# Kernel optimization log

Hardware: AMD Instinct MI355X
Metric: run time of the kernel (lower is better)

## Reference

```python
import jax, jax.numpy as jnp
import numpy as np

D = 64       # link_state_dim
RU = 256     # readout_units
N = 50000    # num_edges (total links)
E = 800000   # number of (main, neighbour) message pairs
K_PATHS = 8
T_STEPS = 3


def setup_inputs() -> dict:
    key = jax.random.key(0)
    ks = jax.random.split(key, 10)
    std = 0.1  # init_weight uses normal(std=0.1) for Linear/GRUCell weights
    return {
        'links_state': jax.random.normal(ks[0], (N, D), dtype=jnp.float32),
        'id_mainEdges': jax.random.randint(ks[1], (E,), 0, N),
        'id_neighbourEdges': jax.random.randint(ks[2], (E,), 0, N),
        'W_msg': std * jax.random.normal(ks[3], (D, 2 * D), dtype=jnp.float32),
        'b_msg': jnp.zeros((D,), jnp.float32),
        'W_ih': std * jax.random.normal(ks[4], (3 * D, D), dtype=jnp.float32),
        'W_hh': std * jax.random.normal(ks[5], (3 * D, D), dtype=jnp.float32),
        'b_ih': jnp.zeros((3 * D,), jnp.float32),
        'b_hh': jnp.zeros((3 * D,), jnp.float32),
        'Wr1': std * jax.random.normal(ks[6], (RU, D), dtype=jnp.float32),
        'br1': jnp.zeros((RU,), jnp.float32),
        'Wr2': std * jax.random.normal(ks[7], (RU, RU), dtype=jnp.float32),
        'br2': jnp.zeros((RU,), jnp.float32),
        'Wr3': std * jax.random.normal(ks[8], (1, RU), dtype=jnp.float32),
        'br3': jnp.zeros((1,), jnp.float32),
        'K': K_PATHS,
        'T': T_STEPS,
        'num_edges': N,
    }


def _gru_cell(x, h, W_ih, W_hh, b_ih, b_hh):
    gi = x @ W_ih.T + b_ih            # [N, 3D]
    gh = h @ W_hh.T + b_hh            # [N, 3D]
    i_r, i_z, i_n = jnp.split(gi, 3, axis=1)
    h_r, h_z, h_n = jnp.split(gh, 3, axis=1)
    r = jax.nn.sigmoid(i_r + h_r)
    z = jax.nn.sigmoid(i_z + h_z)
    n = jnp.tanh(i_n + r * h_n)
    return (1.0 - z) * n + z * h


def reference(links_state, id_mainEdges, id_neighbourEdges, W_msg, b_msg,
              W_ih, W_hh, b_ih, b_hh, Wr1, br1, Wr2, br2, Wr3, br3,
              K, T, num_edges):
    for _ in range(T):  # fixed small message-passing depth
        # gather + concat: [E, 2D]
        cat = jnp.concatenate([links_state[id_mainEdges],
                               links_state[id_neighbourEdges]], axis=1)
        m = jax.nn.selu(cat @ W_msg.T + b_msg)                       # [E, D]
        links_M = jax.ops.segment_sum(m, id_neighbourEdges,
                                      num_segments=num_edges)        # [N, D]
        links_state = _gru_cell(links_M, links_state, W_ih, W_hh, b_ih, b_hh)
    # group edges into K paths (contiguous blocks, per K_paths_ids construction)
    per_path = num_edges // K
    path_ids = jnp.arange(num_edges) // per_path
    k_path_outputs = jax.ops.segment_sum(links_state, path_ids,
                                         num_segments=K)             # [K, D]
    h = jax.nn.selu(k_path_outputs @ Wr1.T + br1)
    h = jax.nn.selu(h @ Wr2.T + br2)
    logits = (h @ Wr3.T + br3).reshape(-1)                           # [K]
    return jax.nn.softmax(logits)  # Categorical probs over K paths
```

## Files before the change

kernel.cpp:

```cpp
#include <hip/hip_runtime.h>
#include <hip/hip_bf16.h>

#define D 64
#define CAP 5120

typedef _Float16 f16;
typedef _Float16 f16x2 __attribute__((ext_vector_type(2)));
typedef _Float16 f16x4 __attribute__((ext_vector_type(4)));
typedef _Float16 f16x8 __attribute__((ext_vector_type(8)));
typedef float f32x16 __attribute__((ext_vector_type(16)));

#define MFMA_F16(a, b, c) __builtin_amdgcn_mfma_f32_32x32x16_f16(a, b, c, 0, 0, 0)

__device__ __forceinline__ float selu_f(float x) {
    const float SC = 1.0507009873554805f;
    const float AL = 1.6732632423543772f;
    return x > 0.f ? SC * x : SC * AL * (__expf(x) - 1.f);
}
__device__ __forceinline__ float sigmoid_f(float x) { return 1.f / (1.f + __expf(-x)); }
__device__ __forceinline__ float tanh_f(float x) {
    float s = x < 0.f ? -1.f : 1.f;
    float t = __expf(-2.f * fabsf(x));
    return s * (1.f - t) / (1.f + t);
}
__device__ __forceinline__ float dot4(float4 a, float4 b, float acc) {
    acc = fmaf(a.x, b.x, acc);
    acc = fmaf(a.y, b.y, acc);
    acc = fmaf(a.z, b.z, acc);
    return fmaf(a.w, b.w, acc);
}
__device__ __forceinline__ f32x16 zero16() {
    f32x16 v;
#pragma unroll
    for (int i = 0; i < 16; ++i) v[i] = 0.f;
    return v;
}

__global__ void __launch_bounds__(256) pack_kernel(const float* __restrict__ Wih,
                                                   const float* __restrict__ Whh,
                                                   const float* __restrict__ Wmsg,
                                                   f16* __restrict__ w16,
                                                   float* __restrict__ kp) {
    int idx = blockIdx.x * 256 + threadIdx.x;
    if (idx < 512) kp[idx] = 0.f;
    int g = idx >> 12;
    int rem = idx & 4095;
    int d = rem >> 6, k0 = rem & 63;
    float v;
    if (g < 3)      v = Wih[(g * 64 + d) * 64 + k0];
    else if (g < 6) v = Whh[((g - 3) * 64 + d) * 64 + k0];
    else            v = Wmsg[d * 128 + (g - 6) * 64 + k0];
    w16[g * 4096 + d * 64 + (k0 ^ ((d & 7) << 3))] = (f16)v;
}

__global__ void __launch_bounds__(256) bucket_kernel(const int* __restrict__ idm,
                                                     const int* __restrict__ idn,
                                                     int* __restrict__ cursor,
                                                     uint2* __restrict__ barr,
                                                     int E, int NBK) {
    __shared__ int hist[256];
    __shared__ int gbase[256];
    __shared__ int loff[256];
    int t = threadIdx.x;
    if (t < NBK) hist[t] = 0;
    __syncthreads();
    int tile = blockIdx.x * 2048;
    int n_[8], m_[8], b_[8];
#pragma unroll
    for (int j = 0; j < 8; ++j) {
        int e = tile + j * 256 + t;
        if (e < E) {
            n_[j] = idn[e];
            m_[j] = idm[e];
            b_[j] = n_[j] >> 8;
            atomicAdd(&hist[b_[j]], 1);
        } else {
            b_[j] = -1;
        }
    }
    __syncthreads();
    if (t < NBK) {
        gbase[t] = hist[t] ? atomicAdd(&cursor[t], hist[t]) : 0;
        loff[t] = 0;
    }
    __syncthreads();
#pragma unroll
    for (int j = 0; j < 8; ++j) {
        if (b_[j] >= 0) {
            int r = atomicAdd(&loff[b_[j]], 1);
            uint2 e;
            e.x = (unsigned)n_[j];
            e.y = (unsigned)m_[j];
            barr[(size_t)b_[j] * CAP + gbase[b_[j]] + r] = e;
        }
    }
}

__global__ void __launch_bounds__(256) csr_kernel(const uint2* __restrict__ barr,
                                                  const int* __restrict__ cursor,
                                                  int* __restrict__ row_start,
                                                  int* __restrict__ csr_src,
                                                  int N, int E) {
    __shared__ int hist[256];
    __shared__ int offs[256];
    __shared__ int curc[256];
    __shared__ int red[256];
    __shared__ int ldsIdm[CAP];
    __shared__ int baseSh;
    int b = blockIdx.x, t = threadIdx.x;
    int cntb = cursor[b];
    red[t] = (t < b) ? cursor[t] : 0;
    __syncthreads();
    for (int off = 128; off > 0; off >>= 1) {
        if (t < off) red[t] += red[t + off];
        __syncthreads();
    }
    if (t == 0) baseSh = red[0];
    hist[t] = 0;
    __syncthreads();
    int base = baseSh;
    for (int i = t; i < cntb; i += 256) {
        int n = (int)(barr[(size_t)b * CAP + i].x) & 255;
        atomicAdd(&hist[n], 1);
    }
    __syncthreads();
    int v0 = hist[t];
    offs[t] = v0;
    __syncthreads();
    for (int off = 1; off < 256; off <<= 1) {
        int v = offs[t];
        int u = (t >= off) ? offs[t - off] : 0;
        __syncthreads();
        offs[t] = v + u;
        __syncthreads();
    }
    int excl = offs[t] - v0;
    curc[t] = excl;
    int node = (b << 8) + t;
    if (node < N) row_start[node] = base + excl;
    if (b == gridDim.x - 1 && t == 0) row_start[N] = E;
    __syncthreads();
    for (int i = t; i < cntb; i += 256) {
        uint2 e = barr[(size_t)b * CAP + i];
        int r = atomicAdd(&curc[e.x & 255], 1);
        ldsIdm[r] = (int)e.y;
    }
    __syncthreads();
    for (int i = t; i < cntb; i += 256) csr_src[base + i] = ldsIdm[i];
}

__global__ void __launch_bounds__(256) gather_kernel(
    const f16* __restrict__ y16, const f16* __restrict__ z16,
    const float* __restrict__ bmsg, const int* __restrict__ row_start,
    const int* __restrict__ csr_src, f16* __restrict__ M16, int N) {
    int lane = threadIdx.x & 63;
    int sub = lane >> 5;
    int d0 = (lane & 31) * 2;
    int wave = blockIdx.x * (blockDim.x >> 6) + (threadIdx.x >> 6);
    int nwaves = gridDim.x * (blockDim.x >> 6);
    float b0 = bmsg[d0], b1 = bmsg[d0 + 1];
    for (int i = wave; i < N; i += nwaves) {
        f16x2 zv = *(const f16x2*)&z16[(size_t)i * 64 + d0];
        float zb0 = (float)zv[0] + b0;
        float zb1 = (float)zv[1] + b1;
        int s1 = row_start[i + 1];
        float m0 = 0.f, m1 = 0.f;
        int s = row_start[i] + sub;
        for (; s + 6 < s1; s += 8) {
            int e0 = csr_src[s],     e1 = csr_src[s + 2];
            int e2 = csr_src[s + 4], e3 = csr_src[s + 6];
            f16x2 v0 = *(const f16x2*)&y16[(size_t)e0 * 64 + d0];
            f16x2 v1 = *(const f16x2*)&y16[(size_t)e1 * 64 + d0];
            f16x2 v2 = *(const f16x2*)&y16[(size_t)e2 * 64 + d0];
            f16x2 v3 = *(const f16x2*)&y16[(size_t)e3 * 64 + d0];
            m0 += selu_f((float)v0[0] + zb0);
            m1 += selu_f((float)v0[1] + zb1);
            m0 += selu_f((float)v1[0] + zb0);
            m1 += selu_f((float)v1[1] + zb1);
            m0 += selu_f((float)v2[0] + zb0);
            m1 += selu_f((float)v2[1] + zb1);
            m0 += selu_f((float)v3[0] + zb0);
            m1 += selu_f((float)v3[1] + zb1);
        }
        for (; s < s1; s += 2) {
            int e0 = csr_src[s];
            f16x2 v0 = *(const f16x2*)&y16[(size_t)e0 * 64 + d0];
            m0 += selu_f((float)v0[0] + zb0);
            m1 += selu_f((float)v0[1] + zb1);
        }
        m0 += __shfl_xor(m0, 32, 64);
        m1 += __shfl_xor(m1, 32, 64);
        if (sub == 0) {
            f16x2 mv; mv[0] = (f16)m0; mv[1] = (f16)m1;
            *(f16x2*)&M16[(size_t)i * 64 + d0] = mv;
        }
    }
}

__global__ void __launch_bounds__(256, 2) yz0_kernel(
    const float* __restrict__ x, const f16* __restrict__ w16,
    f16* __restrict__ y16, f16* __restrict__ z16, int N, int NT) {
    __shared__ __align__(16) f16 wlds[2 * 4096];
    __shared__ __align__(16) f16 xh[64 * 64];
    int t = threadIdx.x;
#pragma unroll
    for (int it = 0; it < 4; ++it) {
        int idx = (it * 256 + t) * 8;
        *(f16x8*)&wlds[idx] = *(const f16x8*)&w16[6 * 4096 + idx];
    }
    int lane = t & 63;
    int w = t >> 6;
    int ng = w >> 1;
    int dh = w & 1;
    int arow = ng * 32 + (lane & 31);
    int arow64 = arow * 64;
    int axor = (arow & 7) << 3;
    int bcol = dh * 32 + (lane & 31);
    int bxor = (bcol & 7) << 3;
    int kg = (lane >> 5) * 8;
    __syncthreads();
    for (int tile = blockIdx.x; tile < NT; tile += gridDim.x) {
        int base = tile * 64;
#pragma unroll
        for (int it = 0; it < 4; ++it) {
            int idx = it * 256 + t;
            int node = idx >> 4, k0 = (idx & 15) * 4;
            int gn = base + node;
            f16x4 v;
            if (gn < N) {
                float4 f4 = *(const float4*)&x[(size_t)gn * 64 + k0];
                v[0] = (f16)f4.x; v[1] = (f16)f4.y; v[2] = (f16)f4.z; v[3] = (f16)f4.w;
            } else {
#pragma unroll
                for (int u = 0; u < 4; ++u) v[u] = (f16)0.f;
            }
            *(f16x4*)&xh[node * 64 + (k0 ^ ((node & 7) << 3))] = v;
        }
        __syncthreads();
        f32x16 aY = zero16(), aZ = zero16();
#pragma unroll
        for (int ks = 0; ks < 4; ++ks) {
            int kb = ks * 16 + kg;
            f16x8 ah = *(const f16x8*)&xh[arow64 + (kb ^ axor)];
            int wof = bcol * 64 + (kb ^ bxor);
            aY = MFMA_F16(ah, *(const f16x8*)&wlds[0 * 4096 + wof], aY);
            aZ = MFMA_F16(ah, *(const f16x8*)&wlds[1 * 4096 + wof], aZ);
        }
#pragma unroll
        for (int r = 0; r < 16; ++r) {
            int rowC = (r & 3) + 8 * (r >> 2) + 4 * (lane >> 5);
            int gn = base + ng * 32 + rowC;
            if (gn < N) {
                size_t o = (size_t)gn * 64 + bcol;
                y16[o] = (f16)aY[r];
                z16[o] = (f16)aZ[r];
            }
        }
        __syncthreads();
    }
}

__global__ void __launch_bounds__(256, 2) gruyz_kernel(
    const f16* __restrict__ M16, const float* __restrict__ hin,
    float* __restrict__ hout,
    const float* __restrict__ bih, const float* __restrict__ bhh,
    const f16* __restrict__ w16, f16* __restrict__ y16, f16* __restrict__ z16,
    int N, int NT, int doYZ) {
    __shared__ __align__(16) f16 wlds[8 * 4096];
    __shared__ __align__(16) f16 xm[64 * 64];
    __shared__ __align__(16) f16 xh[64 * 64];
    int t = threadIdx.x;
#pragma unroll 4
    for (int it = 0; it < 16; ++it) {
        int idx = (it * 256 + t) * 8;
        *(f16x8*)&wlds[idx] = *(const f16x8*)&w16[idx];
    }
    int lane = t & 63;
    int w = t >> 6;
    int ng = w >> 1;
    int dh = w & 1;
    int arow = ng * 32 + (lane & 31);
    int arow64 = arow * 64;
    int axor = (arow & 7) << 3;
    int bcol = dh * 32 + (lane & 31);
    int bxor = (bcol & 7) << 3;
    int kg = (lane >> 5) * 8;
    float bIR = bih[bcol], bIZ = bih[64 + bcol], bIN = bih[128 + bcol];
    float bHR = bhh[bcol], bHZ = bhh[64 + bcol], bHN = bhh[128 + bcol];
    __syncthreads();
    for (int tile = blockIdx.x; tile < NT; tile += gridDim.x) {
        int base = tile * 64;
#pragma unroll
        for (int it = 0; it < 2; ++it) {
            int idx = it * 256 + t;
            int node = idx >> 3, k0 = (idx & 7) * 8;
            int gn = base + node;
            f16x8 v;
            if (gn < N) v = *(const f16x8*)&M16[(size_t)gn * 64 + k0];
            else {
#pragma unroll
            for (int u = 0; u < 8; ++u) v[u] = (f16)0.f;
            }
            *(f16x8*)&xm[node * 64 + (k0 ^ ((node & 7) << 3))] = v;
        }
#pragma unroll
        for (int it = 0; it < 4; ++it) {
            int idx = it * 256 + t;
            int node = idx >> 4, k0 = (idx & 15) * 4;
            int gn = base + node;
            f16x4 v;
            if (gn < N) {
                float4 f4 = *(const float4*)&hin[(size_t)gn * 64 + k0];
                v[0] = (f16)f4.x; v[1] = (f16)f4.y; v[2] = (f16)f4.z; v[3] = (f16)f4.w;
            } else {
#pragma unroll
                for (int u = 0; u < 4; ++u) v[u] = (f16)0.f;
            }
            *(f16x4*)&xh[node * 64 + (k0 ^ ((node & 7) << 3))] = v;
        }
        __syncthreads();

        f32x16 aIR = zero16(), aIZ = zero16(), aIN = zero16();
        f32x16 aHR = zero16(), aHZ = zero16(), aHN = zero16();
#pragma unroll
        for (int ks = 0; ks < 4; ++ks) {
            int kb = ks * 16 + kg;
            f16x8 am = *(const f16x8*)&xm[arow64 + (kb ^ axor)];
            f16x8 ah = *(const f16x8*)&xh[arow64 + (kb ^ axor)];
            int wof = bcol * 64 + (kb ^ bxor);
            aIR = MFMA_F16(am, *(const f16x8*)&wlds[0 * 4096 + wof], aIR);
            aIZ = MFMA_F16(am, *(const f16x8*)&wlds[1 * 4096 + wof], aIZ);
            aIN = MFMA_F16(am, *(const f16x8*)&wlds[2 * 4096 + wof], aIN);
            aHR = MFMA_F16(ah, *(const f16x8*)&wlds[3 * 4096 + wof], aHR);
            aHZ = MFMA_F16(ah, *(const f16x8*)&wlds[4 * 4096 + wof], aHZ);
            aHN = MFMA_F16(ah, *(const f16x8*)&wlds[5 * 4096 + wof], aHN);
        }
        __syncthreads();

#pragma unroll
        for (int r = 0; r < 16; ++r) {
            int rowC = (r & 3) + 8 * (r >> 2) + 4 * (lane >> 5);
            int nodeLocal = ng * 32 + rowC;
            int gn = base + nodeLocal;
            float hnew = 0.f;
            if (gn < N) {
                size_t o = (size_t)gn * 64 + bcol;
                float hold = hin[o];
                float rr = sigmoid_f(aIR[r] + bIR + aHR[r] + bHR);
                float zz = sigmoid_f(aIZ[r] + bIZ + aHZ[r] + bHZ);
                float nn = tanh_f(aIN[r] + bIN + rr * (aHN[r] + bHN));
                hnew = (1.f - zz) * nn + zz * hold;
                hout[o] = hnew;
            }
            if (doYZ) xm[nodeLocal * 64 + (bcol ^ ((rowC & 7) << 3))] = (f16)hnew;
        }
        if (doYZ) {
            __syncthreads();
            f32x16 aY = zero16(), aZ = zero16();
#pragma unroll
            for (int ks = 0; ks < 4; ++ks) {
                int kb = ks * 16 + kg;
                f16x8 ahn2 = *(const f16x8*)&xm[arow64 + (kb ^ axor)];
                int wof = bcol * 64 + (kb ^ bxor);
                aY = MFMA_F16(ahn2, *(const f16x8*)&wlds[6 * 4096 + wof], aY);
                aZ = MFMA_F16(ahn2, *(const f16x8*)&wlds[7 * 4096 + wof], aZ);
            }
#pragma unroll
            for (int r = 0; r < 16; ++r) {
                int rowC = (r & 3) + 8 * (r >> 2) + 4 * (lane >> 5);
                int gn = base + ng * 32 + rowC;
                if (gn < N) {
                    size_t o = (size_t)gn * 64 + bcol;
                    y16[o] = (f16)aY[r];
                    z16[o] = (f16)aZ[r];
                }
            }
        }
        __syncthreads();
    }
}

__global__ void __launch_bounds__(256) pathsum_kernel(const float* __restrict__ h,
                                                      float* __restrict__ kp, int N, int K) {
    int per = N / K;
    int blocksPerPath = gridDim.x / K;
    int p = blockIdx.x / blocksPerPath;
    int c = blockIdx.x % blocksPerPath;
    int d = threadIdx.x & 63;
    int row0 = c * (blockDim.x >> 6) + (threadIdx.x >> 6);
    int stride = blocksPerPath * (blockDim.x >> 6);
    float acc = 0.f;
    for (int r = row0; r < per; r += stride) acc += h[((size_t)p * per + r) * 64 + d];
    __shared__ float red[256];
    red[threadIdx.x] = acc;
    __syncthreads();
    if (threadIdx.x < 64) {
        float s = red[threadIdx.x] + red[64 + threadIdx.x] + red[128 + threadIdx.x] +
                  red[192 + threadIdx.x];
        atomicAdd(&kp[p * 64 + threadIdx.x], s);
    }
}

__global__ void __launch_bounds__(256) readout1_kernel(const float* __restrict__ kp,
                                                       const float* __restrict__ Wr1,
                                                       const float* __restrict__ br1,
                                                       const float* __restrict__ Wr2,
                                                       const float* __restrict__ br2,
                                                       float* __restrict__ h2) {
    int p = blockIdx.x;
    int t = threadIdx.x;
    __shared__ __align__(16) float kps[64];
    __shared__ __align__(16) float h1[256];
    if (t < 64) kps[t] = kp[p * 64 + t];
    __syncthreads();
    float acc = br1[t];
#pragma unroll
    for (int d4 = 0; d4 < 16; ++d4) {
        float4 wv = *(const float4*)&Wr1[t * 64 + d4 * 4];
        float4 kv = *(const float4*)&kps[d4 * 4];
        acc = dot4(wv, kv, acc);
    }
    h1[t] = selu_f(acc);
    __syncthreads();
    float acc2 = br2[t];
#pragma unroll 8
    for (int j4 = 0; j4 < 64; ++j4) {
        float4 wv = *(const float4*)&Wr2[t * 256 + j4 * 4];
        float4 hv = *(const float4*)&h1[j4 * 4];
        acc2 = dot4(wv, hv, acc2);
    }
    h2[p * 256 + t] = selu_f(acc2);
}

__global__ void __launch_bounds__(256) readout2_kernel(const float* __restrict__ h2,
                                                       const float* __restrict__ Wr3,
                                                       const float* __restrict__ br3,
                                                       float* __restrict__ out) {
    __shared__ float red[256];
    __shared__ float lg[8];
    int t = threadIdx.x;
    float w3 = Wr3[t];
    for (int p = 0; p < 8; ++p) {
        red[t] = w3 * h2[p * 256 + t];
        __syncthreads();
        for (int off = 128; off > 0; off >>= 1) {
            if (t < off) red[t] += red[t + off];
            __syncthreads();
        }
        if (t == 0) lg[p] = red[0] + br3[0];
        __syncthreads();
    }
    if (t == 0) {
        float mx = lg[0];
        for (int p = 1; p < 8; ++p) mx = fmaxf(mx, lg[p]);
        float s = 0.f, e[8];
        for (int p = 0; p < 8; ++p) {
            e[p] = expf(lg[p] - mx);
            s += e[p];
        }
        for (int p = 0; p < 8; ++p) out[p] = e[p] / s;
    }
}

extern "C" void kernel_launch(void* const* d_in, const int* in_sizes, int n_in,
                              void* d_out, int out_size, void* d_ws, size_t ws_size,
                              hipStream_t stream) {
    const float* links_state = (const float*)d_in[0];
    const int* idm = (const int*)d_in[1];
    const int* idn = (const int*)d_in[2];
    const float* Wmsg = (const float*)d_in[3];
    const float* bmsg = (const float*)d_in[4];
    const float* Wih = (const float*)d_in[5];
    const float* Whh = (const float*)d_in[6];
    const float* bih = (const float*)d_in[7];
    const float* bhh = (const float*)d_in[8];
    const float* Wr1 = (const float*)d_in[9];
    const float* br1 = (const float*)d_in[10];
    const float* Wr2 = (const float*)d_in[11];
    const float* br2 = (const float*)d_in[12];
    const float* Wr3 = (const float*)d_in[13];
    const float* br3 = (const float*)d_in[14];

    const int N = in_sizes[0] / D;
    const int E = in_sizes[1];
    const int K = 8, T = 3;
    const int NBK = (N + 255) >> 8;
    const int NT = (N + 63) / 64;

    float* ws = (float*)d_ws;
    size_t nd = (size_t)N * D;
    float* cur = ws;
    f16* y16 = (f16*)(ws + nd);
    f16* z16 = y16 + nd;
    f16* M16 = z16 + nd;
    float* kp = (float*)(M16 + nd);
    float* h2 = kp + 512;
    f16* w16 = (f16*)(h2 + 2048);
    uint2* barr = (uint2*)(w16 + 32768);
    int* ibase = (int*)(barr + (size_t)NBK * CAP);
    int* cursor = ibase;
    int* row_start = ibase + 256;
    int* csr_src = row_start + N + 1;

    hipMemsetAsync(cursor, 0, 256 * sizeof(int), stream);
    bucket_kernel<<<dim3((E + 2047) / 2048), dim3(256), 0, stream>>>(idm, idn, cursor, barr,
                                                                     E, NBK);
    csr_kernel<<<dim3(NBK), dim3(256), 0, stream>>>(barr, cursor, row_start, csr_src, N, E);
    pack_kernel<<<dim3(128), dim3(256), 0, stream>>>(Wih, Whh, Wmsg, w16, kp);

    yz0_kernel<<<dim3(512), dim3(256), 0, stream>>>(links_state, w16, y16, z16, N, NT);
    for (int t = 0; t < T; ++t) {
        gather_kernel<<<dim3(2048), dim3(256), 0, stream>>>(y16, z16, bmsg, row_start,
                                                            csr_src, M16, N);
        gruyz_kernel<<<dim3(512), dim3(256), 0, stream>>>(
            M16, (t == 0) ? links_state : cur, cur, bih, bhh, w16, y16, z16, N, NT,
            t < T - 1 ? 1 : 0);
    }

    pathsum_kernel<<<dim3(256), dim3(256), 0, stream>>>(cur, kp, N, K);
    readout1_kernel<<<dim3(8), dim3(256), 0, stream>>>(kp, Wr1, br1, Wr2, br2, h2);
    readout2_kernel<<<dim3(1), dim3(256), 0, stream>>>(h2, Wr3, br3, (float*)d_out);
}
```

Before: 228.2 us.

## Merge setup, path-sum and readout kernels to cut launch count

Weight packing now runs as extra blocks of the bucket kernel, and the yz0 projection runs as extra blocks of the CSR-build kernel. The path sum moves into the last GRU step through per-tile LDS atomics followed by global atomics. The two readout kernels become one, where the last block to finish does the softmax, using a counter and threadfence. This removes several small launches and a full reread of the final state. The cost is more global atomics, a last-block handshake, and larger LDS use in the merged CSR/yz0 kernel, which may lower occupancy.

After: 215.5 us. -5.5%, faster.

```diff
diff --git a/kernel.cpp b/kernel.cpp
--- a/kernel.cpp
+++ b/kernel.cpp
@@ -36,32 +36,31 @@
     return v;
 }
 
-__global__ void __launch_bounds__(256) pack_kernel(const float* __restrict__ Wih,
-                                                   const float* __restrict__ Whh,
-                                                   const float* __restrict__ Wmsg,
-                                                   f16* __restrict__ w16,
-                                                   float* __restrict__ kp) {
-    int idx = blockIdx.x * 256 + threadIdx.x;
-    if (idx < 512) kp[idx] = 0.f;
-    int g = idx >> 12;
-    int rem = idx & 4095;
-    int d = rem >> 6, k0 = rem & 63;
-    float v;
-    if (g < 3)      v = Wih[(g * 64 + d) * 64 + k0];
-    else if (g < 6) v = Whh[((g - 3) * 64 + d) * 64 + k0];
-    else            v = Wmsg[d * 128 + (g - 6) * 64 + k0];
-    w16[g * 4096 + d * 64 + (k0 ^ ((d & 7) << 3))] = (f16)v;
-}
-
-__global__ void __launch_bounds__(256) bucket_kernel(const int* __restrict__ idm,
-                                                     const int* __restrict__ idn,
-                                                     int* __restrict__ cursor,
-                                                     uint2* __restrict__ barr,
-                                                     int E, int NBK) {
+__global__ void __launch_bounds__(256) bucketpack_kernel(
+    const int* __restrict__ idm, const int* __restrict__ idn,
+    int* __restrict__ cursor, uint2* __restrict__ barr,
+    const float* __restrict__ Wih, const float* __restrict__ Whh,
+    const float* __restrict__ Wmsg, f16* __restrict__ w16,
+    float* __restrict__ kp, int* __restrict__ rdcnt,
+    int E, int NBK, int NBB) {
     __shared__ int hist[256];
     __shared__ int gbase[256];
     __shared__ int loff[256];
     int t = threadIdx.x;
+    if ((int)blockIdx.x >= NBB) {
+        int idx = ((int)blockIdx.x - NBB) * 256 + t;
+        if (idx < 512) kp[idx] = 0.f;
+        if (idx == 0) *rdcnt = 0;
+        int g = idx >> 12;
+        int rem = idx & 4095;
+        int d = rem >> 6, k0 = rem & 63;
+        float v;
+        if (g < 3)      v = Wih[(g * 64 + d) * 64 + k0];
+        else if (g < 6) v = Whh[((g - 3) * 64 + d) * 64 + k0];
+        else            v = Wmsg[d * 128 + (g - 6) * 64 + k0];
+        w16[g * 4096 + d * 64 + (k0 ^ ((d & 7) << 3))] = (f16)v;
+        return;
+    }
     if (t < NBK) hist[t] = 0;
     __syncthreads();
     int tile = blockIdx.x * 2048;
@@ -96,57 +95,120 @@
     }
 }
 
-__global__ void __launch_bounds__(256) csr_kernel(const uint2* __restrict__ barr,
-                                                  const int* __restrict__ cursor,
-                                                  int* __restrict__ row_start,
-                                                  int* __restrict__ csr_src,
-                                                  int N, int E) {
+__global__ void __launch_bounds__(256) csryz0_kernel(
+    const uint2* __restrict__ barr, const int* __restrict__ cursor,
+    int* __restrict__ row_start, int* __restrict__ csr_src,
+    const float* __restrict__ x, const f16* __restrict__ w16,
+    f16* __restrict__ y16, f16* __restrict__ z16,
+    int N, int E, int NT, int NBK, int YZGRID) {
     __shared__ int hist[256];
     __shared__ int offs[256];
     __shared__ int curc[256];
     __shared__ int red[256];
     __shared__ int ldsIdm[CAP];
     __shared__ int baseSh;
-    int b = blockIdx.x, t = threadIdx.x;
-    int cntb = cursor[b];
-    red[t] = (t < b) ? cursor[t] : 0;
-    __syncthreads();
-    for (int off = 128; off > 0; off >>= 1) {
-        if (t < off) red[t] += red[t + off];
-        __syncthreads();
-    }
-    if (t == 0) baseSh = red[0];
-    hist[t] = 0;
-    __syncthreads();
-    int base = baseSh;
-    for (int i = t; i < cntb; i += 256) {
-        int n = (int)(barr[(size_t)b * CAP + i].x) & 255;
-        atomicAdd(&hist[n], 1);
-    }
-    __syncthreads();
-    int v0 = hist[t];
-    offs[t] = v0;
-    __syncthreads();
-    for (int off = 1; off < 256; off <<= 1) {
-        int v = offs[t];
-        int u = (t >= off) ? offs[t - off] : 0;
-        __syncthreads();
-        offs[t] = v + u;
-        __syncthreads();
-    }
-    int excl = offs[t] - v0;
-    curc[t] = excl;
-    int node = (b << 8) + t;
-    if (node < N) row_start[node] = base + excl;
-    if (b == gridDim.x - 1 && t == 0) row_start[N] = E;
-    __syncthreads();
-    for (int i = t; i < cntb; i += 256) {
-        uint2 e = barr[(size_t)b * CAP + i];
-        int r = atomicAdd(&curc[e.x & 255], 1);
-        ldsIdm[r] = (int)e.y;
-    }
-    __syncthreads();
-    for (int i = t; i < cntb; i += 256) csr_src[base + i] = ldsIdm[i];
+    __shared__ __align__(16) f16 wlds[2 * 4096];
+    __shared__ __align__(16) f16 xh[64 * 64];
+    int t = threadIdx.x;
+    if ((int)blockIdx.x < NBK) {
+        int b = blockIdx.x;
+        int cntb = cursor[b];
+        red[t] = (t < b) ? cursor[t] : 0;
+        __syncthreads();
+        for (int off = 128; off > 0; off >>= 1) {
+            if (t < off) red[t] += red[t + off];
+            __syncthreads();
+        }
+        if (t == 0) baseSh = red[0];
+        hist[t] = 0;
+        __syncthreads();
+        int base = baseSh;
+        for (int i = t; i < cntb; i += 256) {
+            int n = (int)(barr[(size_t)b * CAP + i].x) & 255;
+            atomicAdd(&hist[n], 1);
+        }
+        __syncthreads();
+        int v0 = hist[t];
+        offs[t] = v0;
+        __syncthreads();
+        for (int off = 1; off < 256; off <<= 1) {
+            int v = offs[t];
+            int u = (t >= off) ? offs[t - off] : 0;
+            __syncthreads();
+            offs[t] = v + u;
+            __syncthreads();
+        }
+        int excl = offs[t] - v0;
+        curc[t] = excl;
+        int node = (b << 8) + t;
+        if (node < N) row_start[node] = base + excl;
+        if (b == NBK - 1 && t == 0) row_start[N] = E;
+        __syncthreads();
+        for (int i = t; i < cntb; i += 256) {
+            uint2 e = barr[(size_t)b * CAP + i];
+            int r = atomicAdd(&curc[e.x & 255], 1);
+            ldsIdm[r] = (int)e.y;
+        }
+        __syncthreads();
+        for (int i = t; i < cntb; i += 256) csr_src[base + i] = ldsIdm[i];
+        return;
+    }
+    int yb = (int)blockIdx.x - NBK;
+#pragma unroll
+    for (int it = 0; it < 4; ++it) {
+        int idx = (it * 256 + t) * 8;
+        *(f16x8*)&wlds[idx] = *(const f16x8*)&w16[6 * 4096 + idx];
+    }
+    int lane = t & 63;
+    int w = t >> 6;
+    int ng = w >> 1;
+    int dh = w & 1;
+    int arow = ng * 32 + (lane & 31);
+    int arow64 = arow * 64;
+    int axor = (arow & 7) << 3;
+    int bcol = dh * 32 + (lane & 31);
+    int bxor = (bcol & 7) << 3;
+    int kg = (lane >> 5) * 8;
+    __syncthreads();
+    for (int tile = yb; tile < NT; tile += YZGRID) {
+        int base = tile * 64;
+#pragma unroll
+        for (int it = 0; it < 4; ++it) {
+            int idx = it * 256 + t;
+            int node = idx >> 4, k0 = (idx & 15) * 4;
+            int gn = base + node;
+            f16x4 v;
+            if (gn < N) {
+                float4 f4 = *(const float4*)&x[(size_t)gn * 64 + k0];
+                v[0] = (f16)f4.x; v[1] = (f16)f4.y; v[2] = (f16)f4.z; v[3] = (f16)f4.w;
+            } else {
+#pragma unroll
+                for (int u = 0; u < 4; ++u) v[u] = (f16)0.f;
+            }
+            *(f16x4*)&xh[node * 64 + (k0 ^ ((node & 7) << 3))] = v;
+        }
+        __syncthreads();
+        f32x16 aY = zero16(), aZ = zero16();
+#pragma unroll
+        for (int ks = 0; ks < 4; ++ks) {
+            int kb = ks * 16 + kg;
+            f16x8 ah = *(const f16x8*)&xh[arow64 + (kb ^ axor)];
+            int wof = bcol * 64 + (kb ^ bxor);
+            aY = MFMA_F16(ah, *(const f16x8*)&wlds[0 * 4096 + wof], aY);
+            aZ = MFMA_F16(ah, *(const f16x8*)&wlds[1 * 4096 + wof], aZ);
+        }
+#pragma unroll
+        for (int r = 0; r < 16; ++r) {
+            int rowC = (r & 3) + 8 * (r >> 2) + 4 * (lane >> 5);
+            int gn = base + ng * 32 + rowC;
+            if (gn < N) {
+                size_t o = (size_t)gn * 64 + bcol;
+                y16[o] = (f16)aY[r];
+                z16[o] = (f16)aZ[r];
+            }
+        }
+        __syncthreads();
+    }
 }
 
 __global__ void __launch_bounds__(256) gather_kernel(
@@ -197,75 +259,12 @@
     }
 }
 
-__global__ void __launch_bounds__(256, 2) yz0_kernel(
-    const float* __restrict__ x, const f16* __restrict__ w16,
-    f16* __restrict__ y16, f16* __restrict__ z16, int N, int NT) {
-    __shared__ __align__(16) f16 wlds[2 * 4096];
-    __shared__ __align__(16) f16 xh[64 * 64];
-    int t = threadIdx.x;
-#pragma unroll
-    for (int it = 0; it < 4; ++it) {
-        int idx = (it * 256 + t) * 8;
-        *(f16x8*)&wlds[idx] = *(const f16x8*)&w16[6 * 4096 + idx];
-    }
-    int lane = t & 63;
-    int w = t >> 6;
-    int ng = w >> 1;
-    int dh = w & 1;
-    int arow = ng * 32 + (lane & 31);
-    int arow64 = arow * 64;
-    int axor = (arow & 7) << 3;
-    int bcol = dh * 32 + (lane & 31);
-    int bxor = (bcol & 7) << 3;
-    int kg = (lane >> 5) * 8;
-    __syncthreads();
-    for (int tile = blockIdx.x; tile < NT; tile += gridDim.x) {
-        int base = tile * 64;
-#pragma unroll
-        for (int it = 0; it < 4; ++it) {
-            int idx = it * 256 + t;
-            int node = idx >> 4, k0 = (idx & 15) * 4;
-            int gn = base + node;
-            f16x4 v;
-            if (gn < N) {
-                float4 f4 = *(const float4*)&x[(size_t)gn * 64 + k0];
-                v[0] = (f16)f4.x; v[1] = (f16)f4.y; v[2] = (f16)f4.z; v[3] = (f16)f4.w;
-            } else {
-#pragma unroll
-                for (int u = 0; u < 4; ++u) v[u] = (f16)0.f;
-            }
-            *(f16x4*)&xh[node * 64 + (k0 ^ ((node & 7) << 3))] = v;
-        }
-        __syncthreads();
-        f32x16 aY = zero16(), aZ = zero16();
-#pragma unroll
-        for (int ks = 0; ks < 4; ++ks) {
-            int kb = ks * 16 + kg;
-            f16x8 ah = *(const f16x8*)&xh[arow64 + (kb ^ axor)];
-            int wof = bcol * 64 + (kb ^ bxor);
-            aY = MFMA_F16(ah, *(const f16x8*)&wlds[0 * 4096 + wof], aY);
-            aZ = MFMA_F16(ah, *(const f16x8*)&wlds[1 * 4096 + wof], aZ);
-        }
-#pragma unroll
-        for (int r = 0; r < 16; ++r) {
-            int rowC = (r & 3) + 8 * (r >> 2) + 4 * (lane >> 5);
-            int gn = base + ng * 32 + rowC;
-            if (gn < N) {
-                size_t o = (size_t)gn * 64 + bcol;
-                y16[o] = (f16)aY[r];
-                z16[o] = (f16)aZ[r];
-            }
-        }
-        __syncthreads();
-    }
-}
-
 __global__ void __launch_bounds__(256, 2) gruyz_kernel(
     const f16* __restrict__ M16, const float* __restrict__ hin,
     float* __restrict__ hout,
     const float* __restrict__ bih, const float* __restrict__ bhh,
     const f16* __restrict__ w16, f16* __restrict__ y16, f16* __restrict__ z16,
-    int N, int NT, int doYZ) {
+    float* __restrict__ kp, int N, int NT, int PER, int doYZ) {
     __shared__ __align__(16) f16 wlds[8 * 4096];
     __shared__ __align__(16) f16 xm[64 * 64];
     __shared__ __align__(16) f16 xh[64 * 64];
@@ -287,6 +286,7 @@
     int kg = (lane >> 5) * 8;
     float bIR = bih[bcol], bIZ = bih[64 + bcol], bIN = bih[128 + bcol];
     float bHR = bhh[bcol], bHZ = bhh[64 + bcol], bHN = bhh[128 + bcol];
+    float* pathbuf = (float*)xm;
     __syncthreads();
     for (int tile = blockIdx.x; tile < NT; tile += gridDim.x) {
         int base = tile * 64;
@@ -299,7 +299,7 @@
             if (gn < N) v = *(const f16x8*)&M16[(size_t)gn * 64 + k0];
             else {
 #pragma unroll
-            for (int u = 0; u < 8; ++u) v[u] = (f16)0.f;
+                for (int u = 0; u < 8; ++u) v[u] = (f16)0.f;
             }
             *(f16x8*)&xm[node * 64 + (k0 ^ ((node & 7) << 3))] = v;
         }
@@ -337,13 +337,20 @@
         }
         __syncthreads();
 
+        int pbase = base / PER;
+        int boundary = (pbase + 1) * PER;
+        if (!doYZ) {
+            if (t < 128) pathbuf[t] = 0.f;
+            __syncthreads();
+        }
 #pragma unroll
         for (int r = 0; r < 16; ++r) {
             int rowC = (r & 3) + 8 * (r >> 2) + 4 * (lane >> 5);
             int nodeLocal = ng * 32 + rowC;
             int gn = base + nodeLocal;
             float hnew = 0.f;
-            if (gn < N) {
+            bool valid = gn < N;
+            if (valid) {
                 size_t o = (size_t)gn * 64 + bcol;
                 float hold = hin[o];
                 float rr = sigmoid_f(aIR[r] + bIR + aHR[r] + bHR);
@@ -352,7 +359,12 @@
                 hnew = (1.f - zz) * nn + zz * hold;
                 hout[o] = hnew;
             }
-            if (doYZ) xm[nodeLocal * 64 + (bcol ^ ((rowC & 7) << 3))] = (f16)hnew;
+            if (doYZ) {
+                xm[nodeLocal * 64 + (bcol ^ ((rowC & 7) << 3))] = (f16)hnew;
+            } else if (valid) {
+                int pidx = (gn >= boundary) ? 1 : 0;
+                atomicAdd(&pathbuf[pidx * 64 + bcol], hnew);
+            }
         }
         if (doYZ) {
             __syncthreads();
@@ -375,42 +387,29 @@
                     z16[o] = (f16)aZ[r];
                 }
             }
-        }
-        __syncthreads();
-    }
-}
-
-__global__ void __launch_bounds__(256) pathsum_kernel(const float* __restrict__ h,
-                                                      float* __restrict__ kp, int N, int K) {
-    int per = N / K;
-    int blocksPerPath = gridDim.x / K;
-    int p = blockIdx.x / blocksPerPath;
-    int c = blockIdx.x % blocksPerPath;
-    int d = threadIdx.x & 63;
-    int row0 = c * (blockDim.x >> 6) + (threadIdx.x >> 6);
-    int stride = blocksPerPath * (blockDim.x >> 6);
-    float acc = 0.f;
-    for (int r = row0; r < per; r += stride) acc += h[((size_t)p * per + r) * 64 + d];
-    __shared__ float red[256];
-    red[threadIdx.x] = acc;
-    __syncthreads();
-    if (threadIdx.x < 64) {
-        float s = red[threadIdx.x] + red[64 + threadIdx.x] + red[128 + threadIdx.x] +
-                  red[192 + threadIdx.x];
-        atomicAdd(&kp[p * 64 + threadIdx.x], s);
-    }
-}
-
-__global__ void __launch_bounds__(256) readout1_kernel(const float* __restrict__ kp,
-                                                       const float* __restrict__ Wr1,
-                                                       const float* __restrict__ br1,
-                                                       const float* __restrict__ Wr2,
-                                                       const float* __restrict__ br2,
-                                                       float* __restrict__ h2) {
+        } else {
+            __syncthreads();
+            if (t < 128) {
+                int p = pbase + (t >> 6);
+                float v = pathbuf[t];
+                if (p < 8 && v != 0.f) atomicAdd(&kp[p * 64 + (t & 63)], v);
+            }
+        }
+        __syncthreads();
+    }
+}
+
+__global__ void __launch_bounds__(256) readout_kernel(
+    const float* __restrict__ kp, const float* __restrict__ Wr1,
+    const float* __restrict__ br1, const float* __restrict__ Wr2,
+    const float* __restrict__ br2, const float* __restrict__ Wr3,
+    const float* __restrict__ br3, float* __restrict__ lgbuf,
+    int* __restrict__ rdcnt, float* __restrict__ out) {
     int p = blockIdx.x;
     int t = threadIdx.x;
     __shared__ __align__(16) float kps[64];
     __shared__ __align__(16) float h1[256];
+    __shared__ float red[256];
     if (t < 64) kps[t] = kp[p * 64 + t];
     __syncthreads();
     float acc = br1[t];
@@ -429,36 +428,31 @@
         float4 hv = *(const float4*)&h1[j4 * 4];
         acc2 = dot4(wv, hv, acc2);
     }
-    h2[p * 256 + t] = selu_f(acc2);
-}
-
-__global__ void __launch_bounds__(256) readout2_kernel(const float* __restrict__ h2,
-                                                       const float* __restrict__ Wr3,
-                                                       const float* __restrict__ br3,
-                                                       float* __restrict__ out) {
-    __shared__ float red[256];
-    __shared__ float lg[8];
-    int t = threadIdx.x;
-    float w3 = Wr3[t];
-    for (int p = 0; p < 8; ++p) {
-        red[t] = w3 * h2[p * 256 + t];
-        __syncthreads();
-        for (int off = 128; off > 0; off >>= 1) {
-            if (t < off) red[t] += red[t + off];
-            __syncthreads();
-        }
-        if (t == 0) lg[p] = red[0] + br3[0];
+    float h2v = selu_f(acc2);
+    red[t] = Wr3[t] * h2v;
+    __syncthreads();
+    for (int off = 128; off > 0; off >>= 1) {
+        if (t < off) red[t] += red[t + off];
         __syncthreads();
     }
     if (t == 0) {
-        float mx = lg[0];
-        for (int p = 1; p < 8; ++p) mx = fmaxf(mx, lg[p]);
-        float s = 0.f, e[8];
-        for (int p = 0; p < 8; ++p) {
-            e[p] = expf(lg[p] - mx);
-            s += e[p];
-        }
-        for (int p = 0; p < 8; ++p) out[p] = e[p] / s;
+        float logit = red[0] + br3[0];
+        atomicExch(&lgbuf[p], logit);
+        __threadfence();
+        int old = atomicAdd(rdcnt, 1);
+        if (old == 7) {
+            float lg[8];
+#pragma unroll
+            for (int j = 0; j < 8; ++j) lg[j] = atomicAdd(&lgbuf[j], 0.f);
+            float mx = lg[0];
+            for (int j = 1; j < 8; ++j) mx = fmaxf(mx, lg[j]);
+            float s = 0.f, e[8];
+            for (int j = 0; j < 8; ++j) {
+                e[j] = __expf(lg[j] - mx);
+                s += e[j];
+            }
+            for (int j = 0; j < 8; ++j) out[j] = e[j] / s;
+        }
     }
 }
 
@@ -485,7 +479,9 @@
     const int E = in_sizes[1];
     const int K = 8, T = 3;
     const int NBK = (N + 255) >> 8;
+    const int NBB = (E + 2047) / 2048;
     const int NT = (N + 63) / 64;
+    const int PER = N / K;
 
     float* ws = (float*)d_ws;
     size_t nd = (size_t)N * D;
@@ -494,8 +490,9 @@
     f16* z16 = y16 + nd;
     f16* M16 = z16 + nd;
     float* kp = (float*)(M16 + nd);
-    float* h2 = kp + 512;
-    f16* w16 = (f16*)(h2 + 2048);
+    float* lgbuf = kp + 512;
+    int* rdcnt = (int*)(lgbuf + 8);
+    f16* w16 = (f16*)(rdcnt + 8);
     uint2* barr = (uint2*)(w16 + 32768);
     int* ibase = (int*)(barr + (size_t)NBK * CAP);
     int* cursor = ibase;
@@ -503,21 +500,19 @@
     int* csr_src = row_start + N + 1;
 
     hipMemsetAsync(cursor, 0, 256 * sizeof(int), stream);
-    bucket_kernel<<<dim3((E + 2047) / 2048), dim3(256), 0, stream>>>(idm, idn, cursor, barr,
-                                                                     E, NBK);
-    csr_kernel<<<dim3(NBK), dim3(256), 0, stream>>>(barr, cursor, row_start, csr_src, N, E);
-    pack_kernel<<<dim3(128), dim3(256), 0, stream>>>(Wih, Whh, Wmsg, w16, kp);
-
-    yz0_kernel<<<dim3(512), dim3(256), 0, stream>>>(links_state, w16, y16, z16, N, NT);
+    bucketpack_kernel<<<dim3(NBB + 128), dim3(256), 0, stream>>>(
+        idm, idn, cursor, barr, Wih, Whh, Wmsg, w16, kp, rdcnt, E, NBK, NBB);
+    csryz0_kernel<<<dim3(NBK + 512), dim3(256), 0, stream>>>(
+        barr, cursor, row_start, csr_src, links_state, w16, y16, z16, N, E, NT, NBK, 512);
+
     for (int t = 0; t < T; ++t) {
         gather_kernel<<<dim3(2048), dim3(256), 0, stream>>>(y16, z16, bmsg, row_start,
                                                             csr_src, M16, N);
         gruyz_kernel<<<dim3(512), dim3(256), 0, stream>>>(
-            M16, (t == 0) ? links_state : cur, cur, bih, bhh, w16, y16, z16, N, NT,
+            M16, (t == 0) ? links_state : cur, cur, bih, bhh, w16, y16, z16, kp, N, NT, PER,
             t < T - 1 ? 1 : 0);
     }
 
-    pathsum_kernel<<<dim3(256), dim3(256), 0, stream>>>(cur, kp, N, K);
-    readout1_kernel<<<dim3(8), dim3(256), 0, stream>>>(kp, Wr1, br1, Wr2, br2, h2);
-    readout2_kernel<<<dim3(1), dim3(256), 0, stream>>>(h2, Wr3, br3, (float*)d_out);
-}
+    readout_kernel<<<dim3(8), dim3(256), 0, stream>>>(kp, Wr1, br1, Wr2, br2, Wr3, br3,
+                                                      lgbuf, rdcnt, (float*)d_out);
+}
```
